# Kernel optimization log

Hardware: AMD Instinct MI355X
Metric: run time of the kernel (lower is better)

Reference implementation:

```python
import jax, jax.numpy as jnp
import numpy as np

N_NODES = 100000
N_EDGES = 1600000
F_IN, F_HID, F_OUT = 32, 32, 16


def gcn_conv(x, W, b, src, dst):
    """GCNConv: out = D^{-1/2} (A+I) D^{-1/2} X W + b (self-loops already in src/dst)."""
    n = x.shape[0]
    h = x @ W  # [N, F_out]
    deg = jax.ops.segment_sum(jnp.ones(dst.shape[0], x.dtype), dst, num_segments=n)
    dinv = jnp.where(deg > 0, jax.lax.rsqrt(deg), jnp.zeros((), x.dtype))
    coef = dinv[src] * dinv[dst]  # [E_total]
    out = jax.ops.segment_sum(h[src] * coef[:, None], dst, num_segments=n)
    return out + b


def setup_inputs() -> dict:
    key = jax.random.key(0)
    k1, k2, k3, k4, k5, k6, k7 = jax.random.split(key, 7)
    x = jax.random.normal(k1, (N_NODES, F_IN), dtype=jnp.float32)
    edge_index = jax.random.randint(k2, (2, N_EDGES), 0, N_NODES, dtype=jnp.int64)
    s1 = 1.0 / np.sqrt(F_IN)
    s2 = 1.0 / np.sqrt(F_HID)
    W1 = jax.random.uniform(k3, (F_IN, F_HID), jnp.float32, -s1, s1)
    b1 = jax.random.uniform(k4, (F_HID,), jnp.float32, -s1, s1)
    W2 = jax.random.uniform(k5, (F_HID, F_OUT), jnp.float32, -s2, s2)
    b2 = jax.random.uniform(k6, (F_OUT,), jnp.float32, -s2, s2)
    return {"x": x, "edge_index": edge_index, "W1": W1, "b1": b1, "W2": W2, "b2": b2}


def reference(x, edge_index, W1, b1, W2, b2):
    n = x.shape[0]
    loops = jnp.arange(n, dtype=edge_index.dtype)  # GCNConv adds self-loops
    src = jnp.concatenate([edge_index[0], loops])
    dst = jnp.concatenate([edge_index[1], loops])
    h = jnp.tanh(gcn_conv(x, W1, b1, src, dst))
    h = gcn_conv(h, W2, b2, src, dst)
    return h, jax.nn.log_softmax(h, axis=1)
```

## Files before the change

### kernel.cpp

```cpp
#include <hip/hip_runtime.h>
#include <hip/hip_bf16.h>
#include <hip/hip_fp16.h>
#include <math.h>
#include <stdint.h>

#define F_IN  32
#define F_HID 32
#define F_OUT 16
#define NPB     256
#define LOG_NPB 8
#define MAXNB   512
#define BH      512

typedef float floatx2 __attribute__((ext_vector_type(2)));

__device__ inline floatx2 fp8_lo(uint32_t w) {
    return __builtin_amdgcn_cvt_pk_f32_fp8(w, false);
}
__device__ inline floatx2 fp8_hi(uint32_t w) {
    return __builtin_amdgcn_cvt_pk_f32_fp8(w, true);
}
__device__ inline uint32_t pack_fp8x4(float a, float b, float c, float d) {
    uint32_t u = __builtin_amdgcn_cvt_pk_fp8_f32(a, b, 0u, false);
    u = __builtin_amdgcn_cvt_pk_fp8_f32(c, d, u, true);
    return u;
}
__device__ inline floatx2 shflx(floatx2 v, int off) {
    floatx2 r;
    r[0] = __shfl_xor(v[0], off);
    r[1] = __shfl_xor(v[1], off);
    return r;
}

__device__ inline float fexp(float x) {
    return __builtin_amdgcn_exp2f(x * 1.44269504089f);
}
__device__ inline float ftanh(float x) {
    x = fminf(fmaxf(x, -15.f), 15.f);
    float t = __builtin_amdgcn_exp2f(x * 2.88539008178f);
    return (t - 1.0f) * __builtin_amdgcn_rcpf(t + 1.0f);
}

__launch_bounds__(512)
__global__ void k_hist(const int* __restrict__ ei, int ne, int chunk, int nb,
                       int* __restrict__ hist_mat) {
    __shared__ int hist[4][MAXNB];
    int t = threadIdx.x, b = blockIdx.x;
    int rep = t >> 7;
    for (int i = t; i < 4 * MAXNB; i += 512) ((int*)hist)[i] = 0;
    __syncthreads();
    long s = (long)b * chunk;
    long e = s + chunk; if (e > ne) e = ne;
    const int* dstp = ei + ne;
    long i = s + (long)t * 4;
    for (; i + 4 <= e; i += 2048) {
        int4 d = *(const int4*)(dstp + i);
        atomicAdd(&hist[rep][d.x >> LOG_NPB], 1);
        atomicAdd(&hist[rep][d.y >> LOG_NPB], 1);
        atomicAdd(&hist[rep][d.z >> LOG_NPB], 1);
        atomicAdd(&hist[rep][d.w >> LOG_NPB], 1);
    }
    if (i < e)
        for (long j = i; j < e; ++j) atomicAdd(&hist[rep][dstp[j] >> LOG_NPB], 1);
    __syncthreads();
    for (int k = t; k < nb; k += 512)
        hist_mat[(size_t)b * nb + k] = hist[0][k] + hist[1][k] + hist[2][k] + hist[3][k];
}

__launch_bounds__(64)
__global__ void k_colscan(const int* __restrict__ hist_mat, int* __restrict__ off_mat,
                          int* __restrict__ totalG, int nb) {
    int k = blockIdx.x;
    if (k >= nb) return;
    int lane = threadIdx.x;
    int run = 0;
    #pragma unroll
    for (int c = 0; c < BH; c += 64) {
        size_t idx = (size_t)(c + lane) * nb + k;
        int v = hist_mat[idx];
        int inc = v;
        #pragma unroll
        for (int o = 1; o < 64; o <<= 1) {
            int u = __shfl_up(inc, o);
            if (lane >= o) inc += u;
        }
        off_mat[idx] = run + inc - v;
        run += __shfl(inc, 63);
    }
    if (lane == 0) totalG[k] = run;
}

__global__ void k_scanb(const int* __restrict__ totalG, int* __restrict__ boff, int nb) {
    __shared__ int sh[256];
    int t = threadIdx.x;
    int base = t * 2;
    int v[2], s = 0;
    #pragma unroll
    for (int j = 0; j < 2; ++j) {
        v[j] = (base + j < nb) ? totalG[base + j] : 0;
        s += v[j];
    }
    sh[t] = s; __syncthreads();
    for (int o = 1; o < 256; o <<= 1) {
        int u = (t >= o) ? sh[t - o] : 0;
        __syncthreads();
        sh[t] += u;
        __syncthreads();
    }
    int run = sh[t] - s;
    #pragma unroll
    for (int j = 0; j < 2; ++j) {
        int k = base + j;
        if (k < nb) { boff[k] = run; run += v[j]; }
    }
    if (t == 255) boff[nb] = sh[255];
}

__launch_bounds__(512)
__global__ void k_fillc(const int* __restrict__ ei, int ne, int chunk, int nb,
                        const int* __restrict__ off_mat, const int* __restrict__ boff,
                        uint32_t* __restrict__ ebuf) {
    __shared__ int cur[MAXNB];
    int t = threadIdx.x, b = blockIdx.x;
    for (int i = t; i < nb; i += 512)
        cur[i] = off_mat[(size_t)b * nb + i] + boff[i];
    __syncthreads();
    long s = (long)b * chunk;
    long e = s + chunk; if (e > ne) e = ne;
    const int* srcp = ei;
    const int* dstp = ei + ne;
    long i = s + (long)t * 4;
    for (; i + 4 <= e; i += 2048) {
        int4 sv = *(const int4*)(srcp + i);
        int4 dv = *(const int4*)(dstp + i);
        int p0 = atomicAdd(&cur[dv.x >> LOG_NPB], 1);
        ebuf[p0] = (uint32_t)sv.x | ((uint32_t)(dv.x & (NPB - 1)) << 17);
        int p1 = atomicAdd(&cur[dv.y >> LOG_NPB], 1);
        ebuf[p1] = (uint32_t)sv.y | ((uint32_t)(dv.y & (NPB - 1)) << 17);
        int p2 = atomicAdd(&cur[dv.z >> LOG_NPB], 1);
        ebuf[p2] = (uint32_t)sv.z | ((uint32_t)(dv.z & (NPB - 1)) << 17);
        int p3 = atomicAdd(&cur[dv.w >> LOG_NPB], 1);
        ebuf[p3] = (uint32_t)sv.w | ((uint32_t)(dv.w & (NPB - 1)) << 17);
    }
    if (i < e) {
        for (long j = i; j < e; ++j) {
            int sn = srcp[j], dn = dstp[j];
            int p = atomicAdd(&cur[dn >> LOG_NPB], 1);
            ebuf[p] = (uint32_t)sn | ((uint32_t)(dn & (NPB - 1)) << 17);
        }
    }
}

__launch_bounds__(256)
__global__ void k_pass2(const uint32_t* __restrict__ ebuf, const int* __restrict__ boff,
                        const float* __restrict__ x,
                        int* __restrict__ csr, int* __restrict__ off_g,
                        float* __restrict__ dinv, uint32_t* __restrict__ xd,
                        int n, int nb) {
    __shared__ int hist[NPB], scn[NPB], cur[NPB];
    __shared__ float sdi[NPB];
    int b = blockIdx.x, t = threadIdx.x;
    int base = boff[b], end = boff[b + 1];
    int v0 = b << LOG_NPB;
    hist[t] = 0;
    __syncthreads();
    for (int i = base + t; i < end; i += 256)
        atomicAdd(&hist[(ebuf[i] >> 17) & (NPB - 1)], 1);
    __syncthreads();
    int val = hist[t];
    scn[t] = val; __syncthreads();
    for (int o = 1; o < 256; o <<= 1) {
        int u = (t >= o) ? scn[t - o] : 0;
        __syncthreads();
        scn[t] += u;
        __syncthreads();
    }
    int excl = scn[t] - val + base;
    cur[t] = excl;
    int v = v0 + t;
    float d = 0.f;
    if (v < n) {
        off_g[v] = excl;
        d = rsqrtf((float)(val + 1));
        dinv[v] = d;
    }
    sdi[t] = d;
    if (b == nb - 1 && t == 0) off_g[n] = end;
    if (b == nb - 1 && t < 8) xd[(size_t)n * 8 + t] = 0u;
    __syncthreads();
    for (int i = base + t; i < end; i += 256) {
        uint32_t r = ebuf[i];
        int slot = atomicAdd(&cur[(r >> 17) & (NPB - 1)], 1);
        csr[slot] = (int)(r & 0x1FFFF);
    }
    for (int i = t; i < NPB * 8; i += 256) {
        int nl = i >> 3, wp = i & 7;
        int vv = v0 + nl;
        if (vv < n) {
            float4 xx = *(const float4*)(x + (size_t)vv * F_IN + 4 * wp);
            float di = sdi[nl];
            xd[(size_t)vv * 8 + wp] =
                pack_fp8x4(xx.x * di, xx.y * di, xx.z * di, xx.w * di);
        }
    }
}

__launch_bounds__(256)
__global__ void k_agg1(const uint32_t* __restrict__ xd, const int* __restrict__ csr,
                       const int* __restrict__ off_g,
                       const float* __restrict__ dinv, const float* __restrict__ b1,
                       const float* __restrict__ W1, const float* __restrict__ W2,
                       uint32_t* __restrict__ g2, int n) {
    __shared__ float W1s[F_IN * F_HID];
    __shared__ float W2s[F_HID * F_OUT];
    __shared__ float sums[8][F_IN + 1];
    __shared__ float hb[8][F_HID + 1];
    int t = threadIdx.x, wv = t >> 6, lane = t & 63;
    ((float4*)W1s)[t] = ((const float4*)W1)[t];
    if (t < 128) ((float4*)W2s)[t] = ((const float4*)W2)[t];
    if (blockIdx.x == 0 && t < 4) g2[(size_t)n * 4 + t] = 0u;
    int half = lane >> 5, l = lane & 31;
    int v = blockIdx.x * 8 + wv * 2 + half;
    bool act = v < n;
    int q = l & 3, slot = l >> 2;
    floatx2 a0 = {0.f, 0.f}, a1 = {0.f, 0.f}, a2 = {0.f, 0.f}, a3 = {0.f, 0.f};
    if (act) {
        int start = off_g[v], cnt = off_g[v + 1] - start;
        const int* cp = csr + start;
        int i0 = (slot      < cnt) ? cp[slot]      : n;
        int i1 = (slot + 8  < cnt) ? cp[slot + 8]  : n;
        int i2 = (slot + 16 < cnt) ? cp[slot + 16] : n;
        int i3 = (slot + 24 < cnt) ? cp[slot + 24] : n;
        int iS = (slot == 0) ? v : n;
        uint2 w0 = *(const uint2*)(xd + (size_t)i0 * 8 + q * 2);
        uint2 w1 = *(const uint2*)(xd + (size_t)i1 * 8 + q * 2);
        uint2 w2 = *(const uint2*)(xd + (size_t)i2 * 8 + q * 2);
        uint2 w3 = *(const uint2*)(xd + (size_t)i3 * 8 + q * 2);
        uint2 wS = *(const uint2*)(xd + (size_t)iS * 8 + q * 2);
        #define ACC8(W) { a0 += fp8_lo(W.x); a1 += fp8_hi(W.x); \
                          a2 += fp8_lo(W.y); a3 += fp8_hi(W.y); }
        ACC8(w0) ACC8(w1) ACC8(w2) ACC8(w3) ACC8(wS)
        for (int k = slot + 32; k < cnt; k += 8) {
            int s = cp[k];
            uint2 wr = *(const uint2*)(xd + (size_t)s * 8 + q * 2);
            ACC8(wr)
        }
        #undef ACC8
    }
    #pragma unroll
    for (int off = 4; off < 32; off <<= 1) {
        a0 += shflx(a0, off);
        a1 += shflx(a1, off);
        a2 += shflx(a2, off);
        a3 += shflx(a3, off);
    }
    if (slot == 0) {
        float* sp = &sums[wv * 2 + half][q * 8];
        sp[0] = a0[0]; sp[1] = a0[1]; sp[2] = a1[0]; sp[3] = a1[1];
        sp[4] = a2[0]; sp[5] = a2[1]; sp[6] = a3[0]; sp[7] = a3[1];
    }
    __syncthreads();
    if (t < 128) {
        int nl = t >> 4, c2 = (t & 15) * 2;
        int v1 = blockIdx.x * 8 + nl;
        float di = (v1 < n) ? dinv[v1] : 0.f;
        float s0 = 0.f, s1 = 0.f;
        #pragma unroll
        for (int k = 0; k < F_IN; ++k) {
            float sk = sums[nl][k];
            float2 wk = *(const float2*)&W1s[k * F_HID + c2];
            s0 += sk * wk.x;
            s1 += sk * wk.y;
        }
        hb[nl][c2]     = ftanh(s0 * di + b1[c2]);
        hb[nl][c2 + 1] = ftanh(s1 * di + b1[c2 + 1]);
    }
    __syncthreads();
    if (t < 32) {
        int nl = t >> 2, c4 = (t & 3) * 4;
        int v2 = blockIdx.x * 8 + nl;
        float s0 = 0.f, s1 = 0.f, s2 = 0.f, s3 = 0.f;
        #pragma unroll
        for (int k = 0; k < F_HID; ++k) {
            float hk = hb[nl][k];
            float4 wk = *(const float4*)&W2s[k * F_OUT + c4];
            s0 += hk * wk.x; s1 += hk * wk.y;
            s2 += hk * wk.z; s3 += hk * wk.w;
        }
        if (v2 < n) {
            float di = dinv[v2];
            g2[(size_t)v2 * 4 + (c4 >> 2)] =
                pack_fp8x4(s0 * di, s1 * di, s2 * di, s3 * di);
        }
    }
}

__launch_bounds__(256)
__global__ void k_agg2(const uint32_t* __restrict__ g2, const int* __restrict__ csr,
                       const int* __restrict__ off_g,
                       const float* __restrict__ dinv, const float* __restrict__ b2,
                       float* __restrict__ out_h, float* __restrict__ out_ls, int n) {
    int t = threadIdx.x, wv = t >> 6, lane = t & 63;
    int half = lane >> 5, l = lane & 31;
    int v = blockIdx.x * 8 + wv * 2 + half;
    bool act = v < n;
    int q = l & 3, slot = l >> 2;
    floatx2 b0 = {0.f, 0.f}, b1v = {0.f, 0.f};
    if (act) {
        int start = off_g[v], cnt = off_g[v + 1] - start;
        const int* cp = csr + start;
        int i0 = (slot      < cnt) ? cp[slot]      : n;
        int i1 = (slot + 8  < cnt) ? cp[slot + 8]  : n;
        int i2 = (slot + 16 < cnt) ? cp[slot + 16] : n;
        int i3 = (slot + 24 < cnt) ? cp[slot + 24] : n;
        int iS = (slot == 0) ? v : n;
        uint32_t w0 = g2[(size_t)i0 * 4 + q];
        uint32_t w1 = g2[(size_t)i1 * 4 + q];
        uint32_t w2 = g2[(size_t)i2 * 4 + q];
        uint32_t w3 = g2[(size_t)i3 * 4 + q];
        uint32_t wS = g2[(size_t)iS * 4 + q];
        #define ACC4(W) { b0 += fp8_lo(W); b1v += fp8_hi(W); }
        ACC4(w0) ACC4(w1) ACC4(w2) ACC4(w3) ACC4(wS)
        for (int k = slot + 32; k < cnt; k += 8) {
            uint32_t wr = g2[(size_t)cp[k] * 4 + q];
            ACC4(wr)
        }
        #undef ACC4
    }
    #pragma unroll
    for (int off = 4; off < 32; off <<= 1) {
        b0 += shflx(b0, off);
        b1v += shflx(b1v, off);
    }
    if (l < 16) {
        int ch = l;
        int src = (lane & 32) + (ch >> 2);
        float a0 = __shfl(b0[0], src), a1 = __shfl(b0[1], src);
        float a2 = __shfl(b1v[0], src), a3 = __shfl(b1v[1], src);
        float f = (ch & 2) ? ((ch & 1) ? a3 : a2) : ((ch & 1) ? a1 : a0);
        float di = act ? dinv[v] : 0.f;
        float val = f * di + b2[ch];
        float m = val;
        m = fmaxf(m, __shfl_xor(m, 1));
        m = fmaxf(m, __shfl_xor(m, 2));
        m = fmaxf(m, __shfl_xor(m, 4));
        m = fmaxf(m, __shfl_xor(m, 8));
        float S = fexp(val - m);
        S += __shfl_xor(S, 1);
        S += __shfl_xor(S, 2);
        S += __shfl_xor(S, 4);
        S += __shfl_xor(S, 8);
        float L = __builtin_amdgcn_logf(S) * 0.69314718056f + m;
        if (act) {
            out_h[(size_t)v * F_OUT + ch]  = val;
            out_ls[(size_t)v * F_OUT + ch] = val - L;
        }
    }
}

static inline size_t align16(size_t x) { return (x + 15) & ~(size_t)15; }

extern "C" void kernel_launch(void* const* d_in, const int* in_sizes, int n_in,
                              void* d_out, int out_size, void* d_ws, size_t ws_size,
                              hipStream_t stream) {
    const float* x  = (const float*)d_in[0];
    const int*   ei = (const int*)d_in[1];
    const float* W1 = (const float*)d_in[2];
    const float* b1 = (const float*)d_in[3];
    const float* W2 = (const float*)d_in[4];
    const float* b2 = (const float*)d_in[5];

    int n  = in_sizes[0] / F_IN;
    int ne = in_sizes[1] / 2;
    int nb = (n + NPB - 1) / NPB;
    int chunk = (((ne + BH - 1) / BH) + 3) & ~3;

    float* out_h  = (float*)d_out;
    float* out_ls = out_h + (size_t)n * F_OUT;

    char* p = (char*)d_ws;
    float*    dinv     = (float*)p;    p += align16((size_t)n * sizeof(float));
    int*      totalG   = (int*)p;      p += align16(MAXNB * sizeof(int));
    int*      boff     = (int*)p;      p += align16((MAXNB + 4) * sizeof(int));
    int*      off_g    = (int*)p;      p += align16(((size_t)n + 4) * sizeof(int));
    int*      hist_mat = (int*)p;      p += align16((size_t)BH * nb * sizeof(int));
    int*      off_mat  = (int*)p;      p += align16((size_t)BH * nb * sizeof(int));
    uint32_t* ebuf     = (uint32_t*)p; p += align16((size_t)ne * sizeof(uint32_t));
    int*      csr      = (int*)p;      p += align16((size_t)ne * sizeof(int));
    uint32_t* xd       = (uint32_t*)p; p += align16(((size_t)n + 1) * 8 * sizeof(uint32_t));
    uint32_t* g2       = (uint32_t*)p; p += align16(((size_t)n + 1) * 4 * sizeof(uint32_t));

    k_hist   <<<BH, 512, 0, stream>>>(ei, ne, chunk, nb, hist_mat);
    k_colscan<<<nb, 64, 0, stream>>>(hist_mat, off_mat, totalG, nb);
    k_scanb  <<<1, 256, 0, stream>>>(totalG, boff, nb);
    k_fillc  <<<BH, 512, 0, stream>>>(ei, ne, chunk, nb, off_mat, boff, ebuf);
    k_pass2  <<<nb, 256, 0, stream>>>(ebuf, boff, x, csr, off_g, dinv, xd, n, nb);

    k_agg1   <<<(n + 7) / 8, 256, 0, stream>>>(xd, csr, off_g, dinv, b1, W1, W2, g2, n);
    k_agg2   <<<(n + 7) / 8, 256, 0, stream>>>(g2, csr, off_g, dinv, b2, out_h, out_ls, n);
}
```

Baseline: 98.31 us.

## Fuse block scan into fill kernel, widen histogram replicas, persist aggregation grids

Removes the single-block k_scanb launch: every k_fillc block now redundantly scans totalG in shared memory, and block 0 writes boff. The k_hist kernel uses 8 shared histogram replicas instead of 4 to reduce LDS atomic contention. The two aggregation kernels become grid-stride loops over node groups with a capped grid of 2048 blocks, so W1/W2 are loaded into shared memory once per block and reused across groups. The costs are a redundant 512-wide scan in every fill block, and fewer resident blocks available to hide the latency of the gather loads.

After: 106.3 us. 8.1% more time.

```diff
diff --git a/kernel.cpp b/kernel.cpp
--- a/kernel.cpp
+++ b/kernel.cpp
@@ -11,6 +11,7 @@
 #define LOG_NPB 8
 #define MAXNB   512
 #define BH      512
+#define PGRID   2048
 
 typedef float floatx2 __attribute__((ext_vector_type(2)));
 
@@ -44,10 +45,10 @@
 __launch_bounds__(512)
 __global__ void k_hist(const int* __restrict__ ei, int ne, int chunk, int nb,
                        int* __restrict__ hist_mat) {
-    __shared__ int hist[4][MAXNB];
+    __shared__ int hist[8][MAXNB];
     int t = threadIdx.x, b = blockIdx.x;
-    int rep = t >> 7;
-    for (int i = t; i < 4 * MAXNB; i += 512) ((int*)hist)[i] = 0;
+    int rep = t >> 6;
+    for (int i = t; i < 8 * MAXNB; i += 512) ((int*)hist)[i] = 0;
     __syncthreads();
     long s = (long)b * chunk;
     long e = s + chunk; if (e > ne) e = ne;
@@ -63,8 +64,12 @@
     if (i < e)
         for (long j = i; j < e; ++j) atomicAdd(&hist[rep][dstp[j] >> LOG_NPB], 1);
     __syncthreads();
-    for (int k = t; k < nb; k += 512)
-        hist_mat[(size_t)b * nb + k] = hist[0][k] + hist[1][k] + hist[2][k] + hist[3][k];
+    for (int k = t; k < nb; k += 512) {
+        int v = 0;
+        #pragma unroll
+        for (int r = 0; r < 8; ++r) v += hist[r][k];
+        hist_mat[(size_t)b * nb + k] = v;
+    }
 }
 
 __launch_bounds__(64)
@@ -90,40 +95,27 @@
     if (lane == 0) totalG[k] = run;
 }
 
-__global__ void k_scanb(const int* __restrict__ totalG, int* __restrict__ boff, int nb) {
-    __shared__ int sh[256];
-    int t = threadIdx.x;
-    int base = t * 2;
-    int v[2], s = 0;
-    #pragma unroll
-    for (int j = 0; j < 2; ++j) {
-        v[j] = (base + j < nb) ? totalG[base + j] : 0;
-        s += v[j];
-    }
-    sh[t] = s; __syncthreads();
-    for (int o = 1; o < 256; o <<= 1) {
-        int u = (t >= o) ? sh[t - o] : 0;
-        __syncthreads();
-        sh[t] += u;
-        __syncthreads();
-    }
-    int run = sh[t] - s;
-    #pragma unroll
-    for (int j = 0; j < 2; ++j) {
-        int k = base + j;
-        if (k < nb) { boff[k] = run; run += v[j]; }
-    }
-    if (t == 255) boff[nb] = sh[255];
-}
-
 __launch_bounds__(512)
 __global__ void k_fillc(const int* __restrict__ ei, int ne, int chunk, int nb,
-                        const int* __restrict__ off_mat, const int* __restrict__ boff,
-                        uint32_t* __restrict__ ebuf) {
+                        const int* __restrict__ off_mat, const int* __restrict__ totalG,
+                        int* __restrict__ boff, uint32_t* __restrict__ ebuf) {
     __shared__ int cur[MAXNB];
+    __shared__ int sc[512];
     int t = threadIdx.x, b = blockIdx.x;
-    for (int i = t; i < nb; i += 512)
-        cur[i] = off_mat[(size_t)b * nb + i] + boff[i];
+    int tv = (t < nb) ? totalG[t] : 0;
+    sc[t] = tv; __syncthreads();
+    for (int o = 1; o < 512; o <<= 1) {
+        int u = (t >= o) ? sc[t - o] : 0;
+        __syncthreads();
+        sc[t] += u;
+        __syncthreads();
+    }
+    int myboff = sc[t] - tv;
+    if (t < nb) cur[t] = off_mat[(size_t)b * nb + t] + myboff;
+    if (b == 0) {
+        if (t < nb) boff[t] = myboff;
+        if (t == 0) boff[nb] = ne;
+    }
     __syncthreads();
     long s = (long)b * chunk;
     long e = s + chunk; if (e > ne) e = ne;
@@ -210,88 +202,92 @@
                        const int* __restrict__ off_g,
                        const float* __restrict__ dinv, const float* __restrict__ b1,
                        const float* __restrict__ W1, const float* __restrict__ W2,
-                       uint32_t* __restrict__ g2, int n) {
+                       uint32_t* __restrict__ g2, int n, int ngroups) {
     __shared__ float W1s[F_IN * F_HID];
     __shared__ float W2s[F_HID * F_OUT];
-    __shared__ float sums[8][F_IN + 1];
-    __shared__ float hb[8][F_HID + 1];
+    __shared__ float sums[2][8][F_IN + 1];
+    __shared__ float hb[2][8][F_HID + 1];
     int t = threadIdx.x, wv = t >> 6, lane = t & 63;
     ((float4*)W1s)[t] = ((const float4*)W1)[t];
     if (t < 128) ((float4*)W2s)[t] = ((const float4*)W2)[t];
     if (blockIdx.x == 0 && t < 4) g2[(size_t)n * 4 + t] = 0u;
     int half = lane >> 5, l = lane & 31;
-    int v = blockIdx.x * 8 + wv * 2 + half;
-    bool act = v < n;
     int q = l & 3, slot = l >> 2;
-    floatx2 a0 = {0.f, 0.f}, a1 = {0.f, 0.f}, a2 = {0.f, 0.f}, a3 = {0.f, 0.f};
-    if (act) {
-        int start = off_g[v], cnt = off_g[v + 1] - start;
-        const int* cp = csr + start;
-        int i0 = (slot      < cnt) ? cp[slot]      : n;
-        int i1 = (slot + 8  < cnt) ? cp[slot + 8]  : n;
-        int i2 = (slot + 16 < cnt) ? cp[slot + 16] : n;
-        int i3 = (slot + 24 < cnt) ? cp[slot + 24] : n;
-        int iS = (slot == 0) ? v : n;
-        uint2 w0 = *(const uint2*)(xd + (size_t)i0 * 8 + q * 2);
-        uint2 w1 = *(const uint2*)(xd + (size_t)i1 * 8 + q * 2);
-        uint2 w2 = *(const uint2*)(xd + (size_t)i2 * 8 + q * 2);
-        uint2 w3 = *(const uint2*)(xd + (size_t)i3 * 8 + q * 2);
-        uint2 wS = *(const uint2*)(xd + (size_t)iS * 8 + q * 2);
-        #define ACC8(W) { a0 += fp8_lo(W.x); a1 += fp8_hi(W.x); \
-                          a2 += fp8_lo(W.y); a3 += fp8_hi(W.y); }
-        ACC8(w0) ACC8(w1) ACC8(w2) ACC8(w3) ACC8(wS)
-        for (int k = slot + 32; k < cnt; k += 8) {
-            int s = cp[k];
-            uint2 wr = *(const uint2*)(xd + (size_t)s * 8 + q * 2);
-            ACC8(wr)
-        }
-        #undef ACC8
-    }
-    #pragma unroll
-    for (int off = 4; off < 32; off <<= 1) {
-        a0 += shflx(a0, off);
-        a1 += shflx(a1, off);
-        a2 += shflx(a2, off);
-        a3 += shflx(a3, off);
-    }
-    if (slot == 0) {
-        float* sp = &sums[wv * 2 + half][q * 8];
-        sp[0] = a0[0]; sp[1] = a0[1]; sp[2] = a1[0]; sp[3] = a1[1];
-        sp[4] = a2[0]; sp[5] = a2[1]; sp[6] = a3[0]; sp[7] = a3[1];
-    }
-    __syncthreads();
-    if (t < 128) {
-        int nl = t >> 4, c2 = (t & 15) * 2;
-        int v1 = blockIdx.x * 8 + nl;
-        float di = (v1 < n) ? dinv[v1] : 0.f;
-        float s0 = 0.f, s1 = 0.f;
+    int p = 0;
+    for (int g = blockIdx.x; g < ngroups; g += PGRID) {
+        int v = g * 8 + wv * 2 + half;
+        bool act = v < n;
+        floatx2 a0 = {0.f, 0.f}, a1 = {0.f, 0.f}, a2 = {0.f, 0.f}, a3 = {0.f, 0.f};
+        if (act) {
+            int start = off_g[v], cnt = off_g[v + 1] - start;
+            const int* cp = csr + start;
+            int i0 = (slot      < cnt) ? cp[slot]      : n;
+            int i1 = (slot + 8  < cnt) ? cp[slot + 8]  : n;
+            int i2 = (slot + 16 < cnt) ? cp[slot + 16] : n;
+            int i3 = (slot + 24 < cnt) ? cp[slot + 24] : n;
+            int iS = (slot == 0) ? v : n;
+            uint2 w0 = *(const uint2*)(xd + (size_t)i0 * 8 + q * 2);
+            uint2 w1 = *(const uint2*)(xd + (size_t)i1 * 8 + q * 2);
+            uint2 w2 = *(const uint2*)(xd + (size_t)i2 * 8 + q * 2);
+            uint2 w3 = *(const uint2*)(xd + (size_t)i3 * 8 + q * 2);
+            uint2 wS = *(const uint2*)(xd + (size_t)iS * 8 + q * 2);
+            #define ACC8(W) { a0 += fp8_lo(W.x); a1 += fp8_hi(W.x); \
+                              a2 += fp8_lo(W.y); a3 += fp8_hi(W.y); }
+            ACC8(w0) ACC8(w1) ACC8(w2) ACC8(w3) ACC8(wS)
+            for (int k = slot + 32; k < cnt; k += 8) {
+                int s = cp[k];
+                uint2 wr = *(const uint2*)(xd + (size_t)s * 8 + q * 2);
+                ACC8(wr)
+            }
+            #undef ACC8
+        }
         #pragma unroll
-        for (int k = 0; k < F_IN; ++k) {
-            float sk = sums[nl][k];
-            float2 wk = *(const float2*)&W1s[k * F_HID + c2];
-            s0 += sk * wk.x;
-            s1 += sk * wk.y;
-        }
-        hb[nl][c2]     = ftanh(s0 * di + b1[c2]);
-        hb[nl][c2 + 1] = ftanh(s1 * di + b1[c2 + 1]);
-    }
-    __syncthreads();
-    if (t < 32) {
-        int nl = t >> 2, c4 = (t & 3) * 4;
-        int v2 = blockIdx.x * 8 + nl;
-        float s0 = 0.f, s1 = 0.f, s2 = 0.f, s3 = 0.f;
-        #pragma unroll
-        for (int k = 0; k < F_HID; ++k) {
-            float hk = hb[nl][k];
-            float4 wk = *(const float4*)&W2s[k * F_OUT + c4];
-            s0 += hk * wk.x; s1 += hk * wk.y;
-            s2 += hk * wk.z; s3 += hk * wk.w;
-        }
-        if (v2 < n) {
-            float di = dinv[v2];
-            g2[(size_t)v2 * 4 + (c4 >> 2)] =
-                pack_fp8x4(s0 * di, s1 * di, s2 * di, s3 * di);
-        }
+        for (int off = 4; off < 32; off <<= 1) {
+            a0 += shflx(a0, off);
+            a1 += shflx(a1, off);
+            a2 += shflx(a2, off);
+            a3 += shflx(a3, off);
+        }
+        if (slot == 0) {
+            float* sp = &sums[p][wv * 2 + half][q * 8];
+            sp[0] = a0[0]; sp[1] = a0[1]; sp[2] = a1[0]; sp[3] = a1[1];
+            sp[4] = a2[0]; sp[5] = a2[1]; sp[6] = a3[0]; sp[7] = a3[1];
+        }
+        __syncthreads();
+        if (t < 128) {
+            int nl = t >> 4, c2 = (t & 15) * 2;
+            int v1 = g * 8 + nl;
+            float di = (v1 < n) ? dinv[v1] : 0.f;
+            float s0 = 0.f, s1 = 0.f;
+            #pragma unroll
+            for (int k = 0; k < F_IN; ++k) {
+                float sk = sums[p][nl][k];
+                float2 wk = *(const float2*)&W1s[k * F_HID + c2];
+                s0 += sk * wk.x;
+                s1 += sk * wk.y;
+            }
+            hb[p][nl][c2]     = ftanh(s0 * di + b1[c2]);
+            hb[p][nl][c2 + 1] = ftanh(s1 * di + b1[c2 + 1]);
+        }
+        __syncthreads();
+        if (t < 32) {
+            int nl = t >> 2, c4 = (t & 3) * 4;
+            int v2 = g * 8 + nl;
+            float s0 = 0.f, s1 = 0.f, s2 = 0.f, s3 = 0.f;
+            #pragma unroll
+            for (int k = 0; k < F_HID; ++k) {
+                float hk = hb[p][nl][k];
+                float4 wk = *(const float4*)&W2s[k * F_OUT + c4];
+                s0 += hk * wk.x; s1 += hk * wk.y;
+                s2 += hk * wk.z; s3 += hk * wk.w;
+            }
+            if (v2 < n) {
+                float di = dinv[v2];
+                g2[(size_t)v2 * 4 + (c4 >> 2)] =
+                    pack_fp8x4(s0 * di, s1 * di, s2 * di, s3 * di);
+            }
+        }
+        p ^= 1;
     }
 }
 
@@ -299,61 +295,64 @@
 __global__ void k_agg2(const uint32_t* __restrict__ g2, const int* __restrict__ csr,
                        const int* __restrict__ off_g,
                        const float* __restrict__ dinv, const float* __restrict__ b2,
-                       float* __restrict__ out_h, float* __restrict__ out_ls, int n) {
+                       float* __restrict__ out_h, float* __restrict__ out_ls,
+                       int n, int ngroups) {
     int t = threadIdx.x, wv = t >> 6, lane = t & 63;
     int half = lane >> 5, l = lane & 31;
-    int v = blockIdx.x * 8 + wv * 2 + half;
-    bool act = v < n;
     int q = l & 3, slot = l >> 2;
-    floatx2 b0 = {0.f, 0.f}, b1v = {0.f, 0.f};
-    if (act) {
-        int start = off_g[v], cnt = off_g[v + 1] - start;
-        const int* cp = csr + start;
-        int i0 = (slot      < cnt) ? cp[slot]      : n;
-        int i1 = (slot + 8  < cnt) ? cp[slot + 8]  : n;
-        int i2 = (slot + 16 < cnt) ? cp[slot + 16] : n;
-        int i3 = (slot + 24 < cnt) ? cp[slot + 24] : n;
-        int iS = (slot == 0) ? v : n;
-        uint32_t w0 = g2[(size_t)i0 * 4 + q];
-        uint32_t w1 = g2[(size_t)i1 * 4 + q];
-        uint32_t w2 = g2[(size_t)i2 * 4 + q];
-        uint32_t w3 = g2[(size_t)i3 * 4 + q];
-        uint32_t wS = g2[(size_t)iS * 4 + q];
-        #define ACC4(W) { b0 += fp8_lo(W); b1v += fp8_hi(W); }
-        ACC4(w0) ACC4(w1) ACC4(w2) ACC4(w3) ACC4(wS)
-        for (int k = slot + 32; k < cnt; k += 8) {
-            uint32_t wr = g2[(size_t)cp[k] * 4 + q];
-            ACC4(wr)
-        }
-        #undef ACC4
-    }
-    #pragma unroll
-    for (int off = 4; off < 32; off <<= 1) {
-        b0 += shflx(b0, off);
-        b1v += shflx(b1v, off);
-    }
-    if (l < 16) {
-        int ch = l;
-        int src = (lane & 32) + (ch >> 2);
-        float a0 = __shfl(b0[0], src), a1 = __shfl(b0[1], src);
-        float a2 = __shfl(b1v[0], src), a3 = __shfl(b1v[1], src);
-        float f = (ch & 2) ? ((ch & 1) ? a3 : a2) : ((ch & 1) ? a1 : a0);
-        float di = act ? dinv[v] : 0.f;
-        float val = f * di + b2[ch];
-        float m = val;
-        m = fmaxf(m, __shfl_xor(m, 1));
-        m = fmaxf(m, __shfl_xor(m, 2));
-        m = fmaxf(m, __shfl_xor(m, 4));
-        m = fmaxf(m, __shfl_xor(m, 8));
-        float S = fexp(val - m);
-        S += __shfl_xor(S, 1);
-        S += __shfl_xor(S, 2);
-        S += __shfl_xor(S, 4);
-        S += __shfl_xor(S, 8);
-        float L = __builtin_amdgcn_logf(S) * 0.69314718056f + m;
+    for (int g = blockIdx.x; g < ngroups; g += PGRID) {
+        int v = g * 8 + wv * 2 + half;
+        bool act = v < n;
+        floatx2 b0 = {0.f, 0.f}, b1v = {0.f, 0.f};
         if (act) {
-            out_h[(size_t)v * F_OUT + ch]  = val;
-            out_ls[(size_t)v * F_OUT + ch] = val - L;
+            int start = off_g[v], cnt = off_g[v + 1] - start;
+            const int* cp = csr + start;
+            int i0 = (slot      < cnt) ? cp[slot]      : n;
+            int i1 = (slot + 8  < cnt) ? cp[slot + 8]  : n;
+            int i2 = (slot + 16 < cnt) ? cp[slot + 16] : n;
+            int i3 = (slot + 24 < cnt) ? cp[slot + 24] : n;
+            int iS = (slot == 0) ? v : n;
+            uint32_t w0 = g2[(size_t)i0 * 4 + q];
+            uint32_t w1 = g2[(size_t)i1 * 4 + q];
+            uint32_t w2 = g2[(size_t)i2 * 4 + q];
+            uint32_t w3 = g2[(size_t)i3 * 4 + q];
+            uint32_t wS = g2[(size_t)iS * 4 + q];
+            #define ACC4(W) { b0 += fp8_lo(W); b1v += fp8_hi(W); }
+            ACC4(w0) ACC4(w1) ACC4(w2) ACC4(w3) ACC4(wS)
+            for (int k = slot + 32; k < cnt; k += 8) {
+                uint32_t wr = g2[(size_t)cp[k] * 4 + q];
+                ACC4(wr)
+            }
+            #undef ACC4
+        }
+        #pragma unroll
+        for (int off = 4; off < 32; off <<= 1) {
+            b0 += shflx(b0, off);
+            b1v += shflx(b1v, off);
+        }
+        if (l < 16) {
+            int ch = l;
+            int src = (lane & 32) + (ch >> 2);
+            float a0 = __shfl(b0[0], src), a1 = __shfl(b0[1], src);
+            float a2 = __shfl(b1v[0], src), a3 = __shfl(b1v[1], src);
+            float f = (ch & 2) ? ((ch & 1) ? a3 : a2) : ((ch & 1) ? a1 : a0);
+            float di = act ? dinv[v] : 0.f;
+            float val = f * di + b2[ch];
+            float m = val;
+            m = fmaxf(m, __shfl_xor(m, 1));
+            m = fmaxf(m, __shfl_xor(m, 2));
+            m = fmaxf(m, __shfl_xor(m, 4));
+            m = fmaxf(m, __shfl_xor(m, 8));
+            float S = fexp(val - m);
+            S += __shfl_xor(S, 1);
+            S += __shfl_xor(S, 2);
+            S += __shfl_xor(S, 4);
+            S += __shfl_xor(S, 8);
+            float L = __builtin_amdgcn_logf(S) * 0.69314718056f + m;
+            if (act) {
+                out_h[(size_t)v * F_OUT + ch]  = val;
+                out_ls[(size_t)v * F_OUT + ch] = val - L;
+            }
         }
     }
 }
@@ -374,6 +373,7 @@
     int ne = in_sizes[1] / 2;
     int nb = (n + NPB - 1) / NPB;
     int chunk = (((ne + BH - 1) / BH) + 3) & ~3;
+    int ngroups = (n + 7) / 8;
 
     float* out_h  = (float*)d_out;
     float* out_ls = out_h + (size_t)n * F_OUT;
@@ -392,10 +392,10 @@
 
     k_hist   <<<BH, 512, 0, stream>>>(ei, ne, chunk, nb, hist_mat);
     k_colscan<<<nb, 64, 0, stream>>>(hist_mat, off_mat, totalG, nb);
-    k_scanb  <<<1, 256, 0, stream>>>(totalG, boff, nb);
-    k_fillc  <<<BH, 512, 0, stream>>>(ei, ne, chunk, nb, off_mat, boff, ebuf);
+    k_fillc  <<<BH, 512, 0, stream>>>(ei, ne, chunk, nb, off_mat, totalG, boff, ebuf);
     k_pass2  <<<nb, 256, 0, stream>>>(ebuf, boff, x, csr, off_g, dinv, xd, n, nb);
 
-    k_agg1   <<<(n + 7) / 8, 256, 0, stream>>>(xd, csr, off_g, dinv, b1, W1, W2, g2, n);
-    k_agg2   <<<(n + 7) / 8, 256, 0, stream>>>(g2, csr, off_g, dinv, b2, out_h, out_ls, n);
-}
+    int ag = (ngroups < PGRID) ? ngroups : PGRID;
+    k_agg1   <<<ag, 256, 0, stream>>>(xd, csr, off_g, dinv, b1, W1, W2, g2, n, ngroups);
+    k_agg2   <<<ag, 256, 0, stream>>>(g2, csr, off_g, dinv, b2, out_h, out_ls, n, ngroups);
+}
```
